# Optimization experiments

Hardware: AMD Instinct MI355X
Metric: run time of the kernel (lower is better)

Reference implementation:

```python
import jax, jax.numpy as jnp
import numpy as np

B, U, F = 32768, 256, 256  # batch, units, input features
LR = 0.01                  # inner_lr
EPS = 1e-3                 # TF LayerNormalization default epsilon


def _layer_norm(x, gamma, beta):
    m = jnp.mean(x, axis=-1, keepdims=True)
    v = jnp.var(x, axis=-1, keepdims=True)
    return (x - m) * jax.lax.rsqrt(v + EPS) * gamma + beta


def _enc(W1, b1, W2, b2, u):
    # mlp_2 inner encoder: Dense(4U, gelu-exact) -> Dense(U)
    return jax.nn.gelu(u @ W1 + b1, approximate=False) @ W2 + b2


def setup_inputs() -> dict:
    key = jax.random.key(0)
    ks = jax.random.split(key, 12)
    def w(k, shape):
        fan_in = shape[0]
        return jax.random.normal(k, shape, jnp.float32) / np.sqrt(fan_in)
    return {
        "x": jax.random.normal(ks[0], (B, F), jnp.float32),
        "h_prev": jax.random.normal(ks[1], (B, U), jnp.float32),
        "W_phi": w(ks[2], (F + U, U)), "b_phi": jnp.zeros((U,), jnp.float32),
        "W_psi": w(ks[3], (F + U, U)), "b_psi": jnp.zeros((U,), jnp.float32),
        "W1": w(ks[4], (U, 4 * U)), "b1": jnp.zeros((4 * U,), jnp.float32),
        "W2": w(ks[5], (4 * U, U)), "b2": jnp.zeros((U,), jnp.float32),
        "W_g": w(ks[6], (U, U)), "g_bias": jnp.zeros((U,), jnp.float32),
        "ln_gamma": jnp.ones((U,), jnp.float32), "ln_beta": jnp.zeros((U,), jnp.float32),
        "W_h": w(ks[7], (U, U)), "h_bias": jnp.zeros((U,), jnp.float32),
    }


def reference(x, h_prev, W_phi, b_phi, W_psi, b_psi, W1, b1, W2, b2,
              W_g, g_bias, ln_gamma, ln_beta, W_h, h_bias):
    z = jnp.concatenate([x, h_prev], axis=-1)          # [B, F+U]
    phi = z @ W_phi + b_phi                            # [B, U], also the inner target

    def inner_loss(params):
        W1_, b1_, W2_, b2_ = params
        r = _enc(W1_, b1_, W2_, b2_, phi) @ W_g + g_bias
        r = _layer_norm(r, ln_gamma, ln_beta)
        return jnp.mean(jnp.square(r - phi)), r

    params = (W1, b1, W2, b2)
    # inner_iterations = 1: one SGD step on the inner-encoder weights only
    (_, recon), grads = jax.value_and_grad(inner_loss, has_aux=True)(params)
    params = tuple(p - LR * g for p, g in zip(params, grads))

    psi = z @ W_psi + b_psi                            # [B, U]
    feat = _enc(*params, psi) + 0.1 * recon            # updated encoder on psi
    out = feat @ W_h + h_bias                          # new hidden / cell output
    return out
```

## Files before the change

### kernel.cpp

```cpp
#include <hip/hip_runtime.h>
#include <math.h>

#define B_N 32768
#define U_N 256
#define H_N 1024
#define LR_C 0.01f
#define EPS_C 1e-3f

typedef unsigned short ushort_t;
typedef unsigned int uint_t;
using frag8 = __attribute__((ext_vector_type(8))) short;
using f32x4 = __attribute__((ext_vector_type(4))) float;

__device__ __forceinline__ float erf_fast(float y) {
    float ay = fabsf(y);
    float t = __builtin_amdgcn_rcpf(fmaf(0.3275911f, ay, 1.0f));
    float p = fmaf(1.061405429f, t, -1.453152027f);
    p = fmaf(p, t, 1.421413741f);
    p = fmaf(p, t, -0.284496736f);
    p = fmaf(p, t, 0.254829592f);
    p = p * t;
    float e = __expf(-ay * ay);
    float r = fmaf(-p, e, 1.0f);
    return copysignf(r, y);
}
__device__ __forceinline__ float gelu_f(float x) {
    return 0.5f * x * (1.0f + erf_fast(x * 0.7071067811865475f));
}
__device__ __forceinline__ float dgelu_f(float x) {
    float c = 0.5f * (1.0f + erf_fast(x * 0.7071067811865475f));
    float p = 0.3989422804014327f * __expf(-0.5f * x * x);
    return fmaf(x, p, c);
}
__device__ __forceinline__ void gelu_pair(float x, float& g, float& d) {
    float ay = fabsf(x) * 0.7071067811865475f;
    float t = __builtin_amdgcn_rcpf(fmaf(0.3275911f, ay, 1.0f));
    float p = fmaf(1.061405429f, t, -1.453152027f);
    p = fmaf(p, t, 1.421413741f);
    p = fmaf(p, t, -0.284496736f);
    p = fmaf(p, t, 0.254829592f);
    p = p * t;
    float e = __expf(-ay * ay);
    float er = copysignf(fmaf(-p, e, 1.0f), x);
    float c = 0.5f * (1.0f + er);
    g = x * c;
    d = fmaf(x * 0.3989422804014327f, e, c);
}
__device__ __forceinline__ void splitf(float v, ushort_t& h, ushort_t& l) {
    uint_t u = __float_as_uint(v);
    h = (ushort_t)(u >> 16);
    float r = v - __uint_as_float(u & 0xFFFF0000u);
    uint_t ru = __float_as_uint(r);
    l = (ushort_t)((ru + 0x7FFFu + ((ru >> 16) & 1u)) >> 16);
}
__device__ __forceinline__ ushort_t cvt_rne(float v) {
    uint_t u = __float_as_uint(v);
    return (ushort_t)((u + 0x7FFFu + ((u >> 16) & 1u)) >> 16);
}
__device__ __forceinline__ float bf2f(ushort_t u) {
    return __uint_as_float((uint_t)u << 16);
}
__device__ __forceinline__ void unpack2(uint_t pa, uint_t pb, uint_t& hw, uint_t& lw) {
    hw = __builtin_amdgcn_perm(pb, pa, 0x07060302u);
    lw = __builtin_amdgcn_perm(pb, pa, 0x05040100u);
}
__device__ __forceinline__ size_t swz(int n, int k, int K) {
    return (size_t)n * K +
           (size_t)((k & ~31) | ((((k >> 3) & 3) ^ ((n >> 1) & 3)) << 3) | (k & 7));
}
__device__ __forceinline__ void gload16(const ushort_t* g, ushort_t* l) {
    __builtin_amdgcn_global_load_lds(
        (const __attribute__((address_space(1))) void*)g,
        (__attribute__((address_space(3))) void*)l, 16, 0, 0);
}

#define EPI_NONE 0
#define EPI_GELU 1
#define EPI_ADDS 3

#define BEP_P   0
#define BEP_PT  1
#define BEP_A1  2
#define BEP_DAT 3

template<int ACONCAT, int APACK, int EPI, int OPACK>
__global__ __launch_bounds__(256)
void mgemm_k(const float* A, const float* A2, const uint_t* __restrict__ AP,
             const ushort_t* __restrict__ BTh, const ushort_t* __restrict__ BTl,
             const float* __restrict__ bias, const ushort_t* __restrict__ Xr,
             float* C, uint_t* Cp,
             int M, int N, int K)
{
    __shared__ ushort_t Ah[128 * 40], Al[128 * 40];
    __shared__ ushort_t Bh[128 * 32], Bl[128 * 32];
    const int tid = threadIdx.x;
    const int m0 = blockIdx.x * 128, n0 = blockIdx.y * 128;
    const int lane = tid & 63, w = tid >> 6;
    const int wm = (w & 1) * 64, wn = (w >> 1) * 64;
    const int fr = lane & 15, fq = lane >> 4;
    const int sr = tid >> 1;
    const int sk = (tid & 1) * 16;

    f32x4 acc[4][4];
    #pragma unroll
    for (int i = 0; i < 4; i++)
        #pragma unroll
        for (int j = 0; j < 4; j++) acc[i][j] = (f32x4){0.f, 0.f, 0.f, 0.f};

    for (int k0 = 0; k0 < K; k0 += 32) {
        {
            const int r0w = w * 32;
            const size_t so = (size_t)(n0 + r0w + (lane >> 2)) * K + k0 + ((lane & 3) << 3);
            gload16(&BTh[so],                  &Bh[r0w * 32]);
            gload16(&BTh[so + (size_t)16 * K], &Bh[(r0w + 16) * 32]);
            gload16(&BTl[so],                  &Bl[r0w * 32]);
            gload16(&BTl[so + (size_t)16 * K], &Bl[(r0w + 16) * 32]);
        }
        if (APACK) {
            const uint_t* ap = AP + (size_t)(m0 + sr) * K + k0 + sk;
            uint4 p0 = *(const uint4*)(ap);
            uint4 p1 = *(const uint4*)(ap + 4);
            uint4 p2 = *(const uint4*)(ap + 8);
            uint4 p3 = *(const uint4*)(ap + 12);
            uint4 h0, h1, l0, l1;
            unpack2(p0.x, p0.y, h0.x, l0.x); unpack2(p0.z, p0.w, h0.y, l0.y);
            unpack2(p1.x, p1.y, h0.z, l0.z); unpack2(p1.z, p1.w, h0.w, l0.w);
            unpack2(p2.x, p2.y, h1.x, l1.x); unpack2(p2.z, p2.w, h1.y, l1.y);
            unpack2(p3.x, p3.y, h1.z, l1.z); unpack2(p3.z, p3.w, h1.w, l1.w);
            *(uint4*)&Ah[sr * 40 + sk]     = h0;
            *(uint4*)&Ah[sr * 40 + sk + 8] = h1;
            *(uint4*)&Al[sr * 40 + sk]     = l0;
            *(uint4*)&Al[sr * 40 + sk + 8] = l1;
        } else {
            #pragma unroll
            for (int g = 0; g < 2; g++) {
                uint4 qh, qa;
                uint_t ph[4], pl[4];
                #pragma unroll
                for (int c = 0; c < 2; c++) {
                    const int ak = k0 + sk + g * 8 + c * 4;
                    const float* ap;
                    if (ACONCAT) ap = (ak < 256) ? (A + (size_t)(m0 + sr) * 256 + ak)
                                                 : (A2 + (size_t)(m0 + sr) * 256 + (ak - 256));
                    else         ap = A + (size_t)(m0 + sr) * K + ak;
                    float4 v = *(const float4*)ap;
                    ushort_t h0,h1,h2,h3,l0,l1,l2,l3;
                    splitf(v.x,h0,l0); splitf(v.y,h1,l1); splitf(v.z,h2,l2); splitf(v.w,h3,l3);
                    ph[c*2]   = (uint_t)h0 | ((uint_t)h1 << 16);
                    ph[c*2+1] = (uint_t)h2 | ((uint_t)h3 << 16);
                    pl[c*2]   = (uint_t)l0 | ((uint_t)l1 << 16);
                    pl[c*2+1] = (uint_t)l2 | ((uint_t)l3 << 16);
                }
                qh.x = ph[0]; qh.y = ph[1]; qh.z = ph[2]; qh.w = ph[3];
                qa.x = pl[0]; qa.y = pl[1]; qa.z = pl[2]; qa.w = pl[3];
                *(uint4*)&Ah[sr * 40 + sk + g * 8] = qh;
                *(uint4*)&Al[sr * 40 + sk + g * 8] = qa;
            }
        }
        __syncthreads();

        frag8 afh[4], afl[4], bfh[4], bfl[4];
        #pragma unroll
        for (int i = 0; i < 4; i++) {
            const int ar = wm + i * 16 + fr;
            afh[i] = *(frag8*)&Ah[ar * 40 + fq * 8];
            afl[i] = *(frag8*)&Al[ar * 40 + fq * 8];
        }
        #pragma unroll
        for (int j = 0; j < 4; j++) {
            const int br = wn + j * 16 + fr;
            const int bs = br * 32 + ((fq ^ ((br >> 1) & 3)) << 3);
            bfh[j] = *(frag8*)&Bh[bs];
            bfl[j] = *(frag8*)&Bl[bs];
        }
        #pragma unroll
        for (int i = 0; i < 4; i++)
            #pragma unroll
            for (int j = 0; j < 4; j++) {
                acc[i][j] = __builtin_amdgcn_mfma_f32_16x16x32_bf16(afh[i], bfh[j], acc[i][j], 0, 0, 0);
                acc[i][j] = __builtin_amdgcn_mfma_f32_16x16x32_bf16(afh[i], bfl[j], acc[i][j], 0, 0, 0);
                acc[i][j] = __builtin_amdgcn_mfma_f32_16x16x32_bf16(afl[i], bfh[j], acc[i][j], 0, 0, 0);
            }
        __syncthreads();
    }

    float bv[4] = {0.f, 0.f, 0.f, 0.f};
    if (bias != nullptr)
        #pragma unroll
        for (int j = 0; j < 4; j++) bv[j] = bias[n0 + wn + j * 16 + fr];
    #pragma unroll
    for (int i = 0; i < 4; i++)
        #pragma unroll
        for (int j = 0; j < 4; j++) {
            const int col = n0 + wn + j * 16 + fr;
            #pragma unroll
            for (int r = 0; r < 4; r++) {
                const int row = m0 + wm + i * 16 + fq * 4 + r;
                const size_t off = (size_t)row * N + col;
                float c = acc[i][j][r] + bv[j];
                if (EPI == EPI_GELU)      c = gelu_f(c);
                else if (EPI == EPI_ADDS) c = c + 0.1f * bf2f(Xr[off]);
                if (OPACK) {
                    ushort_t h, l;
                    splitf(c, h, l);
                    Cp[off] = ((uint_t)h << 16) | (uint_t)l;
                } else {
                    C[off] = c;
                }
            }
        }
}

template<int ACONCAT, int BEP>
__global__ __launch_bounds__(256)
void bgemm_k(const void* Av, const float* A2f, const ushort_t* __restrict__ BTh,
             const float* __restrict__ bias, const ushort_t* __restrict__ GpIn,
             ushort_t* Crm, ushort_t* Cct, ushort_t* GpOut,
             int M, int N, int K)
{
    __shared__ ushort_t Ah[128 * 40];
    __shared__ ushort_t Bh[128 * 32];
    const int tid = threadIdx.x;
    const int m0 = blockIdx.x * 128, n0 = blockIdx.y * 128;
    const int lane = tid & 63, w = tid >> 6;
    const int wm = (w & 1) * 64, wn = (w >> 1) * 64;
    const int fr = lane & 15, fq = lane >> 4;
    const int sr = tid >> 1;
    const int sk = (tid & 1) * 16;

    f32x4 acc[4][4];
    #pragma unroll
    for (int i = 0; i < 4; i++)
        #pragma unroll
        for (int j = 0; j < 4; j++) acc[i][j] = (f32x4){0.f, 0.f, 0.f, 0.f};

    for (int k0 = 0; k0 < K; k0 += 32) {
        {
            const int r0w = w * 32;
            const size_t so = (size_t)(n0 + r0w + (lane >> 2)) * K + k0 + ((lane & 3) << 3);
            gload16(&BTh[so],                  &Bh[r0w * 32]);
            gload16(&BTh[so + (size_t)16 * K], &Bh[(r0w + 16) * 32]);
        }
        if (ACONCAT) {
            const float* A = (const float*)Av;
            #pragma unroll
            for (int g = 0; g < 2; g++) {
                uint_t ph[4];
                #pragma unroll
                for (int c = 0; c < 2; c++) {
                    const int ak = k0 + sk + g * 8 + c * 4;
                    const float* ap = (ak < 256) ? (A + (size_t)(m0 + sr) * 256 + ak)
                                                 : (A2f + (size_t)(m0 + sr) * 256 + (ak - 256));
                    float4 v = *(const float4*)ap;
                    ph[c*2]   = (uint_t)cvt_rne(v.x) | ((uint_t)cvt_rne(v.y) << 16);
                    ph[c*2+1] = (uint_t)cvt_rne(v.z) | ((uint_t)cvt_rne(v.w) << 16);
                }
                uint4 q; q.x = ph[0]; q.y = ph[1]; q.z = ph[2]; q.w = ph[3];
                *(uint4*)&Ah[sr * 40 + sk + g * 8] = q;
            }
        } else {
            const ushort_t* A = (const ushort_t*)Av;
            const size_t ao = (size_t)(m0 + sr) * K + k0 + sk;
            *(uint4*)&Ah[sr * 40 + sk]     = *(const uint4*)&A[ao];
            *(uint4*)&Ah[sr * 40 + sk + 8] = *(const uint4*)&A[ao + 8];
        }
        __syncthreads();

        frag8 af[4], bf[4];
        #pragma unroll
        for (int i = 0; i < 4; i++) af[i] = *(frag8*)&Ah[(wm + i * 16 + fr) * 40 + fq * 8];
        #pragma unroll
        for (int j = 0; j < 4; j++) {
            const int br = wn + j * 16 + fr;
            bf[j] = *(frag8*)&Bh[br * 32 + ((fq ^ ((br >> 1) & 3)) << 3)];
        }
        #pragma unroll
        for (int i = 0; i < 4; i++)
            #pragma unroll
            for (int j = 0; j < 4; j++)
                acc[i][j] = __builtin_amdgcn_mfma_f32_16x16x32_bf16(af[i], bf[j], acc[i][j], 0, 0, 0);
        __syncthreads();
    }

    float bv[4] = {0.f, 0.f, 0.f, 0.f};
    if (bias != nullptr)
        #pragma unroll
        for (int j = 0; j < 4; j++) bv[j] = bias[n0 + wn + j * 16 + fr];
    #pragma unroll
    for (int i = 0; i < 4; i++)
        #pragma unroll
        for (int j = 0; j < 4; j++) {
            const int col = n0 + wn + j * 16 + fr;
            const int rowb = m0 + wm + i * 16 + fq * 4;
            float v[4];
            #pragma unroll
            for (int r = 0; r < 4; r++) v[r] = acc[i][j][r] + bv[j];
            if (BEP == BEP_A1) {
                ushort_t gc[4];
                #pragma unroll
                for (int r = 0; r < 4; r++) {
                    float g, d;
                    gelu_pair(v[r], g, d);
                    gc[r] = cvt_rne(g);
                    Crm[(size_t)(rowb + r) * N + col] = gc[r];
                    GpOut[(size_t)(rowb + r) * N + col] = cvt_rne(d);
                }
                uint_t p0 = (uint_t)gc[0] | ((uint_t)gc[1] << 16);
                uint_t p1 = (uint_t)gc[2] | ((uint_t)gc[3] << 16);
                *(uint2*)&Cct[(size_t)col * M + rowb] = (uint2){p0, p1};
            } else if (BEP == BEP_DAT) {
                ushort_t dc[4];
                #pragma unroll
                for (int r = 0; r < 4; r++)
                    dc[r] = cvt_rne(v[r] * bf2f(GpIn[(size_t)(rowb + r) * N + col]));
                uint_t p0 = (uint_t)dc[0] | ((uint_t)dc[1] << 16);
                uint_t p1 = (uint_t)dc[2] | ((uint_t)dc[3] << 16);
                *(uint2*)&Cct[(size_t)col * M + rowb] = (uint2){p0, p1};
            } else {
                ushort_t cc[4];
                #pragma unroll
                for (int r = 0; r < 4; r++) {
                    cc[r] = cvt_rne(v[r]);
                    Crm[(size_t)(rowb + r) * N + col] = cc[r];
                }
                if (BEP == BEP_PT) {
                    uint_t p0 = (uint_t)cc[0] | ((uint_t)cc[1] << 16);
                    uint_t p1 = (uint_t)cc[2] | ((uint_t)cc[3] << 16);
                    *(uint2*)&Cct[(size_t)col * M + rowb] = (uint2){p0, p1};
                }
            }
        }
}

__global__ __launch_bounds__(256)
void wgrad_k(const ushort_t* __restrict__ AT, const ushort_t* __restrict__ BTt,
             float* C, int M, int N, int KA, int kofsA, int KB, int kofsB, int KC)
{
    __shared__ ushort_t Ah[128 * 40];
    __shared__ ushort_t Bh[128 * 40];
    const int tid = threadIdx.x;
    const int m0 = blockIdx.x * 128, n0 = blockIdx.y * 128;
    const int kbA = kofsA + blockIdx.z * KC;
    const int kbB = kofsB + blockIdx.z * KC;
    const int lane = tid & 63, w = tid >> 6;
    const int wm = (w & 1) * 64, wn = (w >> 1) * 64;
    const int fr = lane & 15, fq = lane >> 4;
    const int sr = tid >> 1;
    const int sk = (tid & 1) * 16;

    f32x4 acc[4][4];
    #pragma unroll
    for (int i = 0; i < 4; i++)
        #pragma unroll
        for (int j = 0; j < 4; j++) acc[i][j] = (f32x4){0.f, 0.f, 0.f, 0.f};

    for (int k0 = 0; k0 < KC; k0 += 32) {
        const size_t ao = (size_t)(m0 + sr) * KA + kbA + k0 + sk;
        *(uint4*)&Ah[sr * 40 + sk]     = *(const uint4*)&AT[ao];
        *(uint4*)&Ah[sr * 40 + sk + 8] = *(const uint4*)&AT[ao + 8];
        const size_t bo = (size_t)(n0 + sr) * KB + kbB + k0 + sk;
        *(uint4*)&Bh[sr * 40 + sk]     = *(const uint4*)&BTt[bo];
        *(uint4*)&Bh[sr * 40 + sk + 8] = *(const uint4*)&BTt[bo + 8];
        __syncthreads();

        frag8 af[4], bf[4];
        #pragma unroll
        for (int i = 0; i < 4; i++) af[i] = *(frag8*)&Ah[(wm + i * 16 + fr) * 40 + fq * 8];
        #pragma unroll
        for (int j = 0; j < 4; j++) bf[j] = *(frag8*)&Bh[(wn + j * 16 + fr) * 40 + fq * 8];
        #pragma unroll
        for (int i = 0; i < 4; i++)
            #pragma unroll
            for (int j = 0; j < 4; j++)
                acc[i][j] = __builtin_amdgcn_mfma_f32_16x16x32_bf16(af[i], bf[j], acc[i][j], 0, 0, 0);
        __syncthreads();
    }
    #pragma unroll
    for (int i = 0; i < 4; i++)
        #pragma unroll
        for (int j = 0; j < 4; j++) {
            const int col = n0 + wn + j * 16 + fr;
            #pragma unroll
            for (int r = 0; r < 4; r++) {
                const int row = m0 + wm + i * 16 + fq * 4 + r;
                atomicAdd(&C[(size_t)row * N + col], acc[i][j][r]);
            }
        }
}

__global__ __launch_bounds__(256)
void colsumT_k(const ushort_t* __restrict__ T, float* db, int LD, int cols)
{
    const int n = blockIdx.x * 4 + (threadIdx.x >> 6);
    const int lane = threadIdx.x & 63;
    const ushort_t* row = T + (size_t)n * LD;
    float s = 0.f;
    for (int c = lane * 8; c < cols; c += 512) {
        uint4 q = *(const uint4*)&row[c];
        uint_t u[4] = {q.x, q.y, q.z, q.w};
        #pragma unroll
        for (int t = 0; t < 4; t++) {
            s += bf2f((ushort_t)(u[t] & 0xFFFF));
            s += bf2f((ushort_t)(u[t] >> 16));
        }
    }
    #pragma unroll
    for (int o = 32; o > 0; o >>= 1) s += __shfl_xor(s, o);
    if (lane == 0) atomicAdd(&db[n], s);
}

__global__ __launch_bounds__(256)
void ln_bf_k(const ushort_t* r0, const ushort_t* __restrict__ phi,
             const float* __restrict__ gamma, const float* __restrict__ beta,
             ushort_t* recon, ushort_t* dr0)
{
    const int lane = threadIdx.x & 63;
    const int wv = threadIdx.x >> 6;
    const int row = blockIdx.x * 4 + wv;
    const size_t base = (size_t)row * U_N + (lane << 2);

    uint2 xu = *(const uint2*)(r0 + base);
    uint2 pu = *(const uint2*)(phi + base);
    float xs[4] = { bf2f((ushort_t)(xu.x & 0xFFFF)), bf2f((ushort_t)(xu.x >> 16)),
                    bf2f((ushort_t)(xu.y & 0xFFFF)), bf2f((ushort_t)(xu.y >> 16)) };
    float ps[4] = { bf2f((ushort_t)(pu.x & 0xFFFF)), bf2f((ushort_t)(pu.x >> 16)),
                    bf2f((ushort_t)(pu.y & 0xFFFF)), bf2f((ushort_t)(pu.y >> 16)) };
    float s = xs[0] + xs[1] + xs[2] + xs[3];
    float sq = xs[0]*xs[0] + xs[1]*xs[1] + xs[2]*xs[2] + xs[3]*xs[3];
    #pragma unroll
    for (int o = 32; o > 0; o >>= 1) { s += __shfl_xor(s, o); sq += __shfl_xor(sq, o); }
    const float m   = s * (1.0f / U_N);
    const float var = sq * (1.0f / U_N) - m * m;
    const float inv = rsqrtf(var + EPS_C);

    float4 gv = *(const float4*)(gamma + (lane << 2));
    float4 bvv = *(const float4*)(beta + (lane << 2));
    float gs[4] = {gv.x, gv.y, gv.z, gv.w};
    float bs[4] = {bvv.x, bvv.y, bvv.z, bvv.w};
    float rh[4], dh[4], rc[4];
    float s1 = 0.f, s2 = 0.f;
    const float gscale = 2.0f / ((float)B_N * (float)U_N);
    #pragma unroll
    for (int j = 0; j < 4; j++) {
        rh[j] = (xs[j] - m) * inv;
        rc[j] = rh[j] * gs[j] + bs[j];
        float g2 = gscale * (rc[j] - ps[j]);
        dh[j] = g2 * gs[j];
        s1 += dh[j];
        s2 += dh[j] * rh[j];
    }
    #pragma unroll
    for (int o = 32; o > 0; o >>= 1) { s1 += __shfl_xor(s1, o); s2 += __shfl_xor(s2, o); }
    const float mu1 = s1 * (1.0f / U_N);
    const float mu2 = s2 * (1.0f / U_N);
    ushort_t oc[4], dc[4];
    #pragma unroll
    for (int j = 0; j < 4; j++) {
        oc[j] = cvt_rne(rc[j]);
        dc[j] = cvt_rne(inv * (dh[j] - mu1 - rh[j] * mu2));
    }
    *(uint2*)(recon + base) = (uint2){ (uint_t)oc[0] | ((uint_t)oc[1] << 16),
                                       (uint_t)oc[2] | ((uint_t)oc[3] << 16) };
    *(uint2*)(dr0 + base)   = (uint2){ (uint_t)dc[0] | ((uint_t)dc[1] << 16),
                                       (uint_t)dc[2] | ((uint_t)dc[3] << 16) };
}

template<int HASL>
__global__ __launch_bounds__(256)
void tsplit_k(const float* __restrict__ W, ushort_t* __restrict__ Th,
              ushort_t* __restrict__ Tl, int R, int C)
{
    __shared__ float t[64][65];
    const int tid = threadIdx.x;
    const int R0 = blockIdx.x * 64, C0 = blockIdx.y * 64;
    const int c = tid & 63, rb = (tid >> 6) * 16;
    for (int i = 0; i < 16; i++)
        t[rb + i][c] = W[(size_t)(R0 + rb + i) * C + C0 + c];
    __syncthreads();
    const int orr = tid & 63, ob = (tid >> 6) * 16;
    for (int i = 0; i < 16; i++) {
        const int oc = ob + i;
        ushort_t h, l;
        splitf(t[orr][oc], h, l);
        const size_t d = swz(C0 + oc, R0 + orr, R);
        Th[d] = h;
        if (HASL) Tl[d] = l;
    }
}

__global__ __launch_bounds__(256)
void tupd_k(const float* __restrict__ W, const float* __restrict__ dW,
            ushort_t* __restrict__ Th, ushort_t* __restrict__ Tl, int R, int C)
{
    __shared__ float t[64][65];
    const int tid = threadIdx.x;
    const int R0 = blockIdx.x * 64, C0 = blockIdx.y * 64;
    const int c = tid & 63, rb = (tid >> 6) * 16;
    for (int i = 0; i < 16; i++) {
        const size_t o = (size_t)(R0 + rb + i) * C + C0 + c;
        t[rb + i][c] = W[o] - LR_C * dW[o];
    }
    __syncthreads();
    const int orr = tid & 63, ob = (tid >> 6) * 16;
    for (int i = 0; i < 16; i++) {
        const int oc = ob + i;
        ushort_t h, l;
        splitf(t[orr][oc], h, l);
        const size_t d = swz(C0 + oc, R0 + orr, R);
        Th[d] = h;
        Tl[d] = l;
    }
}

__global__ __launch_bounds__(256)
void scvt_k(const float* __restrict__ W, ushort_t* __restrict__ Th, int n4)
{
    const int i = blockIdx.x * 256 + threadIdx.x;
    if (i >= n4) return;
    float4 v = *(const float4*)(W + (size_t)i * 4);
    const int f = i * 4;
    const int row = f >> 8, col = f & 255;
    uint2 ph;
    ph.x = (uint_t)cvt_rne(v.x) | ((uint_t)cvt_rne(v.y) << 16);
    ph.y = (uint_t)cvt_rne(v.z) | ((uint_t)cvt_rne(v.w) << 16);
    *(uint2*)&Th[swz(row, col, 256)] = ph;
}

__global__ __launch_bounds__(256)
void bupd_k(const float* __restrict__ b1, const float* __restrict__ db1,
            const float* __restrict__ b2, const float* __restrict__ db2,
            float* __restrict__ b1u, float* __restrict__ b2u)
{
    const int i = blockIdx.x * 256 + threadIdx.x;
    if (i < H_N) b1u[i] = b1[i] - LR_C * db1[i];
    else if (i < H_N + U_N) b2u[i - H_N] = b2[i - H_N] - LR_C * db2[i - H_N];
}

extern "C" void kernel_launch(void* const* d_in, const int* in_sizes, int n_in,
                              void* d_out, int out_size, void* d_ws, size_t ws_size,
                              hipStream_t stream)
{
    const float* x      = (const float*)d_in[0];
    const float* h_prev = (const float*)d_in[1];
    const float* W_phi  = (const float*)d_in[2];
    const float* b_phi  = (const float*)d_in[3];
    const float* W_psi  = (const float*)d_in[4];
    const float* b_psi  = (const float*)d_in[5];
    const float* W1     = (const float*)d_in[6];
    const float* b1     = (const float*)d_in[7];
    const float* W2     = (const float*)d_in[8];
    const float* b2     = (const float*)d_in[9];
    const float* W_g    = (const float*)d_in[10];
    const float* g_bias = (const float*)d_in[11];
    const float* gamma  = (const float*)d_in[12];
    const float* beta   = (const float*)d_in[13];
    const float* W_h    = (const float*)d_in[14];
    const float* h_bias = (const float*)d_in[15];
    float* out = (float*)d_out;

    const size_t BU = (size_t)B_N * U_N;
    const size_t UH = (size_t)U_N * H_N;

    float* ws  = (float*)d_ws;
    float* dW1 = ws;
    float* db1 = dW1 + UH;
    float* dW2 = db1 + H_N;
    float* db2 = dW2 + UH;
    float* b1u = db2 + U_N;
    float* b2u = b1u + H_N;
    ushort_t* us = (ushort_t*)(((uintptr_t)(b2u + U_N) + 15) & ~(uintptr_t)15);
    ushort_t* WphiT_h = us;
    ushort_t* WpsiT_h = WphiT_h + 131072;     ushort_t* WpsiT_l = WpsiT_h + 131072;
    ushort_t* W1T_h   = WpsiT_l + 131072;
    ushort_t* W2T_h   = W1T_h + 262144;
    ushort_t* W2s_h   = W2T_h + 262144;
    ushort_t* Wgs_h   = W2s_h + 262144;
    ushort_t* WgT_h   = Wgs_h + 65536;
    ushort_t* W1uT_h  = WgT_h + 65536;        ushort_t* W1uT_l = W1uT_h + 262144;
    ushort_t* W2uT_h  = W1uT_l + 262144;      ushort_t* W2uT_l = W2uT_h + 262144;
    ushort_t* WhT_h   = W2uT_l + 262144;      ushort_t* WhT_l  = WhT_h + 65536;
    ushort_t* phi_bf  = WhT_l + 65536;
    ushort_t* phiT_bf = phi_bf + BU;
    ushort_t* recon_bf= phiT_bf + BU;
    ushort_t* chunk0  = recon_bf + BU;
    const size_t P_bytes = (size_t)((char*)chunk0 - (char*)d_ws);

    int GA = 2;
    while (GA < 256 && P_bytes + (size_t)(B_N / GA) * 10240 + (1 << 20) > ws_size) GA *= 2;
    size_t region = (size_t)(B_N / GA) * 10240;
    int GC = 1;
    while (GC < 256) {
        size_t cC = (size_t)(B_N / GC) * 6144;
        size_t r = cC > region ? cC : region;
        if (P_bytes + r + (1 << 20) <= ws_size) { region = r; break; }
        GC *= 2;
    }
    const int BcA = B_N / GA;
    const int BcC = B_N / GC;
    const int KC = (BcA >= 8192) ? 512 : ((BcA >= 1024) ? BcA / 16 : BcA);
    const int Z  = BcA / KC;

    ushort_t* g1  = chunk0;
    ushort_t* gp  = g1  + (size_t)BcA * H_N;
    ushort_t* g1T = gp  + (size_t)BcA * H_N;
    ushort_t* daT = g1T + (size_t)BcA * H_N;
    ushort_t* e_b = daT + (size_t)BcA * H_N;
    ushort_t* r0b = e_b + (size_t)BcA * U_N;
    ushort_t* deb = r0b + (size_t)BcA * U_N;
    ushort_t* deT = deb + (size_t)BcA * U_N;
    uint_t* psi_p  = (uint_t*)chunk0;
    uint_t* h2_p   = psi_p + (size_t)BcC * U_N;
    uint_t* feat_p = h2_p  + (size_t)BcC * H_N;

    hipMemsetAsync(dW1, 0, (2 * UH + H_N + U_N) * sizeof(float), stream);

    dim3 blk(256);
    tsplit_k<0><<<dim3(8, 4),  blk, 0, stream>>>(W_phi, WphiT_h, nullptr, 512, 256);
    tsplit_k<1><<<dim3(8, 4),  blk, 0, stream>>>(W_psi, WpsiT_h, WpsiT_l, 512, 256);
    tsplit_k<0><<<dim3(4, 16), blk, 0, stream>>>(W1, W1T_h, nullptr, 256, 1024);
    tsplit_k<0><<<dim3(16, 4), blk, 0, stream>>>(W2, W2T_h, nullptr, 1024, 256);
    tsplit_k<0><<<dim3(4, 4),  blk, 0, stream>>>(W_g, WgT_h, nullptr, 256, 256);
    tsplit_k<1><<<dim3(4, 4),  blk, 0, stream>>>(W_h, WhT_h, WhT_l, 256, 256);
    scvt_k<<<dim3(256), blk, 0, stream>>>(W2, W2s_h, 65536);
    scvt_k<<<dim3(64),  blk, 0, stream>>>(W_g, Wgs_h, 16384);

    bgemm_k<1, BEP_PT><<<dim3(B_N / 128, 2), blk, 0, stream>>>(
        x, h_prev, WphiT_h, b_phi, nullptr, phi_bf, phiT_bf, nullptr, B_N, U_N, 512);

    for (int c = 0; c < GA; c++) {
        const size_t off = (size_t)c * BcA;
        const ushort_t* phic = phi_bf + off * U_N;
        bgemm_k<0, BEP_A1><<<dim3(BcA / 128, 8), blk, 0, stream>>>(
            phic, nullptr, W1T_h, b1, nullptr, g1, g1T, gp, BcA, H_N, U_N);
        bgemm_k<0, BEP_P><<<dim3(BcA / 128, 2), blk, 0, stream>>>(
            g1, nullptr, W2T_h, b2, nullptr, e_b, nullptr, nullptr, BcA, U_N, H_N);
        bgemm_k<0, BEP_P><<<dim3(BcA / 128, 2), blk, 0, stream>>>(
            e_b, nullptr, WgT_h, g_bias, nullptr, r0b, nullptr, nullptr, BcA, U_N, U_N);
        ln_bf_k<<<dim3(BcA / 4), blk, 0, stream>>>(r0b, phic, gamma, beta,
                                                   recon_bf + off * U_N, r0b);
        bgemm_k<0, BEP_PT><<<dim3(BcA / 128, 2), blk, 0, stream>>>(
            r0b, nullptr, Wgs_h, nullptr, nullptr, deb, deT, nullptr, BcA, U_N, U_N);
        bgemm_k<0, BEP_DAT><<<dim3(BcA / 128, 8), blk, 0, stream>>>(
            deb, nullptr, W2s_h, nullptr, gp, nullptr, daT, nullptr, BcA, H_N, U_N);
        wgrad_k<<<dim3(8, 2, Z), blk, 0, stream>>>(g1T, deT, dW2, H_N, U_N,
                                                   BcA, 0, BcA, 0, KC);
        colsumT_k<<<dim3(U_N / 4), blk, 0, stream>>>(deT, db2, BcA, BcA);
        wgrad_k<<<dim3(2, 8, Z), blk, 0, stream>>>(phiT_bf, daT, dW1, U_N, H_N,
                                                   B_N, (int)off, BcA, 0, KC);
        colsumT_k<<<dim3(H_N / 4), blk, 0, stream>>>(daT, db1, BcA, BcA);
    }

    bupd_k<<<dim3(5), blk, 0, stream>>>(b1, db1, b2, db2, b1u, b2u);
    tupd_k<<<dim3(4, 16), blk, 0, stream>>>(W1, dW1, W1uT_h, W1uT_l, 256, 1024);
    tupd_k<<<dim3(16, 4), blk, 0, stream>>>(W2, dW2, W2uT_h, W2uT_l, 1024, 256);

    for (int c = 0; c < GC; c++) {
        const size_t off = (size_t)c * BcC;
        mgemm_k<1, 0, EPI_NONE, 1><<<dim3(BcC / 128, 2), blk, 0, stream>>>(
            x + off * 256, h_prev + off * U_N, nullptr,
            WpsiT_h, WpsiT_l, b_psi, nullptr,
            nullptr, psi_p, BcC, U_N, 512);
        mgemm_k<0, 1, EPI_GELU, 1><<<dim3(BcC / 128, 8), blk, 0, stream>>>(
            nullptr, nullptr, psi_p,
            W1uT_h, W1uT_l, b1u, nullptr,
            nullptr, h2_p, BcC, H_N, U_N);
        mgemm_k<0, 1, EPI_ADDS, 1><<<dim3(BcC / 128, 2), blk, 0, stream>>>(
            nullptr, nullptr, h2_p,
            W2uT_h, W2uT_l, b2u, recon_bf + off * U_N,
            nullptr, feat_p, BcC, U_N, H_N);
        mgemm_k<0, 1, EPI_NONE, 0><<<dim3(BcC / 128, 2), blk, 0, stream>>>(
            nullptr, nullptr, feat_p,
            WhT_h, WhT_l, h_bias, nullptr,
            out + off * U_N, nullptr, BcC, U_N, U_N);
    }
}
```

Baseline: 873.6 us.

## Load MFMA fragments directly from global memory, bypassing LDS staging

GEMM kernels whose A operand is already bf16 or packed (bgemm, mgemm and wgrad variants) now read MFMA fragments straight from global memory into registers, dropping the LDS tiles and __syncthreads barriers. The concat/float-input GEMMs keep LDS staging as separate kernels. Weight layouts consumed by the direct kernels are written unswizzled to match plain row indexing. This removes LDS traffic and barrier stalls but gives up cross-wave operand sharing through LDS, so each wave issues redundant global/L2 loads with strided 16-byte accesses.

Measured after the change: 1.091 ms. +24.9%, slower.

```diff
diff --git a/kernel.cpp b/kernel.cpp
--- a/kernel.cpp
+++ b/kernel.cpp
@@ -26,11 +26,6 @@
 }
 __device__ __forceinline__ float gelu_f(float x) {
     return 0.5f * x * (1.0f + erf_fast(x * 0.7071067811865475f));
-}
-__device__ __forceinline__ float dgelu_f(float x) {
-    float c = 0.5f * (1.0f + erf_fast(x * 0.7071067811865475f));
-    float p = 0.3989422804014327f * __expf(-0.5f * x * x);
-    return fmaf(x, p, c);
 }
 __device__ __forceinline__ void gelu_pair(float x, float& g, float& d) {
     float ay = fabsf(x) * 0.7071067811865475f;
@@ -83,23 +78,19 @@
 #define BEP_A1  2
 #define BEP_DAT 3
 
-template<int ACONCAT, int APACK, int EPI, int OPACK>
-__global__ __launch_bounds__(256)
-void mgemm_k(const float* A, const float* A2, const uint_t* __restrict__ AP,
+template<int EPI, int OPACK>
+__global__ __launch_bounds__(256)
+void mgemm_d(const uint_t* __restrict__ AP,
              const ushort_t* __restrict__ BTh, const ushort_t* __restrict__ BTl,
              const float* __restrict__ bias, const ushort_t* __restrict__ Xr,
              float* C, uint_t* Cp,
              int M, int N, int K)
 {
-    __shared__ ushort_t Ah[128 * 40], Al[128 * 40];
-    __shared__ ushort_t Bh[128 * 32], Bl[128 * 32];
     const int tid = threadIdx.x;
     const int m0 = blockIdx.x * 128, n0 = blockIdx.y * 128;
     const int lane = tid & 63, w = tid >> 6;
     const int wm = (w & 1) * 64, wn = (w >> 1) * 64;
     const int fr = lane & 15, fq = lane >> 4;
-    const int sr = tid >> 1;
-    const int sk = (tid & 1) * 16;
 
     f32x4 acc[4][4];
     #pragma unroll
@@ -108,70 +99,23 @@
         for (int j = 0; j < 4; j++) acc[i][j] = (f32x4){0.f, 0.f, 0.f, 0.f};
 
     for (int k0 = 0; k0 < K; k0 += 32) {
-        {
-            const int r0w = w * 32;
-            const size_t so = (size_t)(n0 + r0w + (lane >> 2)) * K + k0 + ((lane & 3) << 3);
-            gload16(&BTh[so],                  &Bh[r0w * 32]);
-            gload16(&BTh[so + (size_t)16 * K], &Bh[(r0w + 16) * 32]);
-            gload16(&BTl[so],                  &Bl[r0w * 32]);
-            gload16(&BTl[so + (size_t)16 * K], &Bl[(r0w + 16) * 32]);
-        }
-        if (APACK) {
-            const uint_t* ap = AP + (size_t)(m0 + sr) * K + k0 + sk;
-            uint4 p0 = *(const uint4*)(ap);
+        frag8 afh[4], afl[4], bfh[4], bfl[4];
+        #pragma unroll
+        for (int i = 0; i < 4; i++) {
+            const uint_t* ap = AP + (size_t)(m0 + wm + i * 16 + fr) * K + k0 + fq * 8;
+            uint4 p0 = *(const uint4*)ap;
             uint4 p1 = *(const uint4*)(ap + 4);
-            uint4 p2 = *(const uint4*)(ap + 8);
-            uint4 p3 = *(const uint4*)(ap + 12);
-            uint4 h0, h1, l0, l1;
-            unpack2(p0.x, p0.y, h0.x, l0.x); unpack2(p0.z, p0.w, h0.y, l0.y);
-            unpack2(p1.x, p1.y, h0.z, l0.z); unpack2(p1.z, p1.w, h0.w, l0.w);
-            unpack2(p2.x, p2.y, h1.x, l1.x); unpack2(p2.z, p2.w, h1.y, l1.y);
-            unpack2(p3.x, p3.y, h1.z, l1.z); unpack2(p3.z, p3.w, h1.w, l1.w);
-            *(uint4*)&Ah[sr * 40 + sk]     = h0;
-            *(uint4*)&Ah[sr * 40 + sk + 8] = h1;
-            *(uint4*)&Al[sr * 40 + sk]     = l0;
-            *(uint4*)&Al[sr * 40 + sk + 8] = l1;
-        } else {
-            #pragma unroll
-            for (int g = 0; g < 2; g++) {
-                uint4 qh, qa;
-                uint_t ph[4], pl[4];
-                #pragma unroll
-                for (int c = 0; c < 2; c++) {
-                    const int ak = k0 + sk + g * 8 + c * 4;
-                    const float* ap;
-                    if (ACONCAT) ap = (ak < 256) ? (A + (size_t)(m0 + sr) * 256 + ak)
-                                                 : (A2 + (size_t)(m0 + sr) * 256 + (ak - 256));
-                    else         ap = A + (size_t)(m0 + sr) * K + ak;
-                    float4 v = *(const float4*)ap;
-                    ushort_t h0,h1,h2,h3,l0,l1,l2,l3;
-                    splitf(v.x,h0,l0); splitf(v.y,h1,l1); splitf(v.z,h2,l2); splitf(v.w,h3,l3);
-                    ph[c*2]   = (uint_t)h0 | ((uint_t)h1 << 16);
-                    ph[c*2+1] = (uint_t)h2 | ((uint_t)h3 << 16);
-                    pl[c*2]   = (uint_t)l0 | ((uint_t)l1 << 16);
-                    pl[c*2+1] = (uint_t)l2 | ((uint_t)l3 << 16);
-                }
-                qh.x = ph[0]; qh.y = ph[1]; qh.z = ph[2]; qh.w = ph[3];
-                qa.x = pl[0]; qa.y = pl[1]; qa.z = pl[2]; qa.w = pl[3];
-                *(uint4*)&Ah[sr * 40 + sk + g * 8] = qh;
-                *(uint4*)&Al[sr * 40 + sk + g * 8] = qa;
-            }
-        }
-        __syncthreads();
-
-        frag8 afh[4], afl[4], bfh[4], bfl[4];
-        #pragma unroll
-        for (int i = 0; i < 4; i++) {
-            const int ar = wm + i * 16 + fr;
-            afh[i] = *(frag8*)&Ah[ar * 40 + fq * 8];
-            afl[i] = *(frag8*)&Al[ar * 40 + fq * 8];
+            uint4 h, l;
+            unpack2(p0.x, p0.y, h.x, l.x); unpack2(p0.z, p0.w, h.y, l.y);
+            unpack2(p1.x, p1.y, h.z, l.z); unpack2(p1.z, p1.w, h.w, l.w);
+            afh[i] = *(frag8*)&h;
+            afl[i] = *(frag8*)&l;
         }
         #pragma unroll
         for (int j = 0; j < 4; j++) {
-            const int br = wn + j * 16 + fr;
-            const int bs = br * 32 + ((fq ^ ((br >> 1) & 3)) << 3);
-            bfh[j] = *(frag8*)&Bh[bs];
-            bfl[j] = *(frag8*)&Bl[bs];
+            const size_t bo = (size_t)(n0 + wn + j * 16 + fr) * K + k0 + fq * 8;
+            bfh[j] = *(const frag8*)&BTh[bo];
+            bfl[j] = *(const frag8*)&BTl[bo];
         }
         #pragma unroll
         for (int i = 0; i < 4; i++)
@@ -181,7 +125,6 @@
                 acc[i][j] = __builtin_amdgcn_mfma_f32_16x16x32_bf16(afh[i], bfl[j], acc[i][j], 0, 0, 0);
                 acc[i][j] = __builtin_amdgcn_mfma_f32_16x16x32_bf16(afl[i], bfh[j], acc[i][j], 0, 0, 0);
             }
-        __syncthreads();
     }
 
     float bv[4] = {0.f, 0.f, 0.f, 0.f};
@@ -195,7 +138,7 @@
             const int col = n0 + wn + j * 16 + fr;
             #pragma unroll
             for (int r = 0; r < 4; r++) {
-                const int row = m0 + wm + i * 16 + fq * 4 + r;
+                const int row = m0 + wm + i * 16 + (lane >> 4) * 4 + r;
                 const size_t off = (size_t)row * N + col;
                 float c = acc[i][j][r] + bv[j];
                 if (EPI == EPI_GELU)      c = gelu_f(c);
@@ -211,15 +154,16 @@
         }
 }
 
-template<int ACONCAT, int BEP>
-__global__ __launch_bounds__(256)
-void bgemm_k(const void* Av, const float* A2f, const ushort_t* __restrict__ BTh,
-             const float* __restrict__ bias, const ushort_t* __restrict__ GpIn,
-             ushort_t* Crm, ushort_t* Cct, ushort_t* GpOut,
+template<int OPACK>
+__global__ __launch_bounds__(256)
+void mgemm_c(const float* A, const float* A2,
+             const ushort_t* __restrict__ BTh, const ushort_t* __restrict__ BTl,
+             const float* __restrict__ bias,
+             float* C, uint_t* Cp,
              int M, int N, int K)
 {
-    __shared__ ushort_t Ah[128 * 40];
-    __shared__ ushort_t Bh[128 * 32];
+    __shared__ ushort_t Ah[128 * 40], Al[128 * 40];
+    __shared__ ushort_t Bh[128 * 32], Bl[128 * 32];
     const int tid = threadIdx.x;
     const int m0 = blockIdx.x * 128, n0 = blockIdx.y * 128;
     const int lane = tid & 63, w = tid >> 6;
@@ -240,46 +184,115 @@
             const size_t so = (size_t)(n0 + r0w + (lane >> 2)) * K + k0 + ((lane & 3) << 3);
             gload16(&BTh[so],                  &Bh[r0w * 32]);
             gload16(&BTh[so + (size_t)16 * K], &Bh[(r0w + 16) * 32]);
-        }
-        if (ACONCAT) {
-            const float* A = (const float*)Av;
-            #pragma unroll
-            for (int g = 0; g < 2; g++) {
-                uint_t ph[4];
-                #pragma unroll
-                for (int c = 0; c < 2; c++) {
-                    const int ak = k0 + sk + g * 8 + c * 4;
-                    const float* ap = (ak < 256) ? (A + (size_t)(m0 + sr) * 256 + ak)
-                                                 : (A2f + (size_t)(m0 + sr) * 256 + (ak - 256));
-                    float4 v = *(const float4*)ap;
-                    ph[c*2]   = (uint_t)cvt_rne(v.x) | ((uint_t)cvt_rne(v.y) << 16);
-                    ph[c*2+1] = (uint_t)cvt_rne(v.z) | ((uint_t)cvt_rne(v.w) << 16);
-                }
-                uint4 q; q.x = ph[0]; q.y = ph[1]; q.z = ph[2]; q.w = ph[3];
-                *(uint4*)&Ah[sr * 40 + sk + g * 8] = q;
-            }
-        } else {
-            const ushort_t* A = (const ushort_t*)Av;
-            const size_t ao = (size_t)(m0 + sr) * K + k0 + sk;
-            *(uint4*)&Ah[sr * 40 + sk]     = *(const uint4*)&A[ao];
-            *(uint4*)&Ah[sr * 40 + sk + 8] = *(const uint4*)&A[ao + 8];
+            gload16(&BTl[so],                  &Bl[r0w * 32]);
+            gload16(&BTl[so + (size_t)16 * K], &Bl[(r0w + 16) * 32]);
+        }
+        #pragma unroll
+        for (int g = 0; g < 2; g++) {
+            uint4 qh, qa;
+            uint_t ph[4], pl[4];
+            #pragma unroll
+            for (int c = 0; c < 2; c++) {
+                const int ak = k0 + sk + g * 8 + c * 4;
+                const float* ap = (ak < 256) ? (A + (size_t)(m0 + sr) * 256 + ak)
+                                             : (A2 + (size_t)(m0 + sr) * 256 + (ak - 256));
+                float4 v = *(const float4*)ap;
+                ushort_t h0,h1,h2,h3,l0,l1,l2,l3;
+                splitf(v.x,h0,l0); splitf(v.y,h1,l1); splitf(v.z,h2,l2); splitf(v.w,h3,l3);
+                ph[c*2]   = (uint_t)h0 | ((uint_t)h1 << 16);
+                ph[c*2+1] = (uint_t)h2 | ((uint_t)h3 << 16);
+                pl[c*2]   = (uint_t)l0 | ((uint_t)l1 << 16);
+                pl[c*2+1] = (uint_t)l2 | ((uint_t)l3 << 16);
+            }
+            qh.x = ph[0]; qh.y = ph[1]; qh.z = ph[2]; qh.w = ph[3];
+            qa.x = pl[0]; qa.y = pl[1]; qa.z = pl[2]; qa.w = pl[3];
+            *(uint4*)&Ah[sr * 40 + sk + g * 8] = qh;
+            *(uint4*)&Al[sr * 40 + sk + g * 8] = qa;
         }
         __syncthreads();
 
-        frag8 af[4], bf[4];
-        #pragma unroll
-        for (int i = 0; i < 4; i++) af[i] = *(frag8*)&Ah[(wm + i * 16 + fr) * 40 + fq * 8];
+        frag8 afh[4], afl[4], bfh[4], bfl[4];
+        #pragma unroll
+        for (int i = 0; i < 4; i++) {
+            const int ar = wm + i * 16 + fr;
+            afh[i] = *(frag8*)&Ah[ar * 40 + fq * 8];
+            afl[i] = *(frag8*)&Al[ar * 40 + fq * 8];
+        }
         #pragma unroll
         for (int j = 0; j < 4; j++) {
             const int br = wn + j * 16 + fr;
-            bf[j] = *(frag8*)&Bh[br * 32 + ((fq ^ ((br >> 1) & 3)) << 3)];
-        }
+            const int bs = br * 32 + ((fq ^ ((br >> 1) & 3)) << 3);
+            bfh[j] = *(frag8*)&Bh[bs];
+            bfl[j] = *(frag8*)&Bl[bs];
+        }
+        #pragma unroll
+        for (int i = 0; i < 4; i++)
+            #pragma unroll
+            for (int j = 0; j < 4; j++) {
+                acc[i][j] = __builtin_amdgcn_mfma_f32_16x16x32_bf16(afh[i], bfh[j], acc[i][j], 0, 0, 0);
+                acc[i][j] = __builtin_amdgcn_mfma_f32_16x16x32_bf16(afh[i], bfl[j], acc[i][j], 0, 0, 0);
+                acc[i][j] = __builtin_amdgcn_mfma_f32_16x16x32_bf16(afl[i], bfh[j], acc[i][j], 0, 0, 0);
+            }
+        __syncthreads();
+    }
+
+    float bv[4] = {0.f, 0.f, 0.f, 0.f};
+    if (bias != nullptr)
+        #pragma unroll
+        for (int j = 0; j < 4; j++) bv[j] = bias[n0 + wn + j * 16 + fr];
+    #pragma unroll
+    for (int i = 0; i < 4; i++)
+        #pragma unroll
+        for (int j = 0; j < 4; j++) {
+            const int col = n0 + wn + j * 16 + fr;
+            #pragma unroll
+            for (int r = 0; r < 4; r++) {
+                const int row = m0 + wm + i * 16 + fq * 4 + r;
+                const size_t off = (size_t)row * N + col;
+                float c = acc[i][j][r] + bv[j];
+                if (OPACK) {
+                    ushort_t h, l;
+                    splitf(c, h, l);
+                    Cp[off] = ((uint_t)h << 16) | (uint_t)l;
+                } else {
+                    C[off] = c;
+                }
+            }
+        }
+}
+
+template<int BEP>
+__global__ __launch_bounds__(256)
+void bgemm_d(const ushort_t* __restrict__ A, const ushort_t* __restrict__ BTh,
+             const float* __restrict__ bias, const ushort_t* __restrict__ GpIn,
+             ushort_t* Crm, ushort_t* Cct, ushort_t* GpOut,
+             int M, int N, int K)
+{
+    const int tid = threadIdx.x;
+    const int m0 = blockIdx.x * 128, n0 = blockIdx.y * 128;
+    const int lane = tid & 63, w = tid >> 6;
+    const int wm = (w & 1) * 64, wn = (w >> 1) * 64;
+    const int fr = lane & 15, fq = lane >> 4;
+
+    f32x4 acc[4][4];
+    #pragma unroll
+    for (int i = 0; i < 4; i++)
+        #pragma unroll
+        for (int j = 0; j < 4; j++) acc[i][j] = (f32x4){0.f, 0.f, 0.f, 0.f};
+
+    for (int k0 = 0; k0 < K; k0 += 32) {
+        frag8 af[4], bf[4];
+        #pragma unroll
+        for (int i = 0; i < 4; i++)
+            af[i] = *(const frag8*)&A[(size_t)(m0 + wm + i * 16 + fr) * K + k0 + fq * 8];
+        #pragma unroll
+        for (int j = 0; j < 4; j++)
+            bf[j] = *(const frag8*)&BTh[(size_t)(n0 + wn + j * 16 + fr) * K + k0 + fq * 8];
         #pragma unroll
         for (int i = 0; i < 4; i++)
             #pragma unroll
             for (int j = 0; j < 4; j++)
                 acc[i][j] = __builtin_amdgcn_mfma_f32_16x16x32_bf16(af[i], bf[j], acc[i][j], 0, 0, 0);
-        __syncthreads();
     }
 
     float bv[4] = {0.f, 0.f, 0.f, 0.f};
@@ -332,12 +345,97 @@
         }
 }
 
+template<int BEP>
+__global__ __launch_bounds__(256)
+void bgemm_c(const float* A, const float* A2f, const ushort_t* __restrict__ BTh,
+             const float* __restrict__ bias,
+             ushort_t* Crm, ushort_t* Cct,
+             int M, int N, int K)
+{
+    __shared__ ushort_t Ah[128 * 40];
+    __shared__ ushort_t Bh[128 * 32];
+    const int tid = threadIdx.x;
+    const int m0 = blockIdx.x * 128, n0 = blockIdx.y * 128;
+    const int lane = tid & 63, w = tid >> 6;
+    const int wm = (w & 1) * 64, wn = (w >> 1) * 64;
+    const int fr = lane & 15, fq = lane >> 4;
+    const int sr = tid >> 1;
+    const int sk = (tid & 1) * 16;
+
+    f32x4 acc[4][4];
+    #pragma unroll
+    for (int i = 0; i < 4; i++)
+        #pragma unroll
+        for (int j = 0; j < 4; j++) acc[i][j] = (f32x4){0.f, 0.f, 0.f, 0.f};
+
+    for (int k0 = 0; k0 < K; k0 += 32) {
+        {
+            const int r0w = w * 32;
+            const size_t so = (size_t)(n0 + r0w + (lane >> 2)) * K + k0 + ((lane & 3) << 3);
+            gload16(&BTh[so],                  &Bh[r0w * 32]);
+            gload16(&BTh[so + (size_t)16 * K], &Bh[(r0w + 16) * 32]);
+        }
+        #pragma unroll
+        for (int g = 0; g < 2; g++) {
+            uint_t ph[4];
+            #pragma unroll
+            for (int c = 0; c < 2; c++) {
+                const int ak = k0 + sk + g * 8 + c * 4;
+                const float* ap = (ak < 256) ? (A + (size_t)(m0 + sr) * 256 + ak)
+                                             : (A2f + (size_t)(m0 + sr) * 256 + (ak - 256));
+                float4 v = *(const float4*)ap;
+                ph[c*2]   = (uint_t)cvt_rne(v.x) | ((uint_t)cvt_rne(v.y) << 16);
+                ph[c*2+1] = (uint_t)cvt_rne(v.z) | ((uint_t)cvt_rne(v.w) << 16);
+            }
+            uint4 q; q.x = ph[0]; q.y = ph[1]; q.z = ph[2]; q.w = ph[3];
+            *(uint4*)&Ah[sr * 40 + sk + g * 8] = q;
+        }
+        __syncthreads();
+
+        frag8 af[4], bf[4];
+        #pragma unroll
+        for (int i = 0; i < 4; i++) af[i] = *(frag8*)&Ah[(wm + i * 16 + fr) * 40 + fq * 8];
+        #pragma unroll
+        for (int j = 0; j < 4; j++) {
+            const int br = wn + j * 16 + fr;
+            bf[j] = *(frag8*)&Bh[br * 32 + ((fq ^ ((br >> 1) & 3)) << 3)];
+        }
+        #pragma unroll
+        for (int i = 0; i < 4; i++)
+            #pragma unroll
+            for (int j = 0; j < 4; j++)
+                acc[i][j] = __builtin_amdgcn_mfma_f32_16x16x32_bf16(af[i], bf[j], acc[i][j], 0, 0, 0);
+        __syncthreads();
+    }
+
+    float bv[4] = {0.f, 0.f, 0.f, 0.f};
+    if (bias != nullptr)
+        #pragma unroll
+        for (int j = 0; j < 4; j++) bv[j] = bias[n0 + wn + j * 16 + fr];
+    #pragma unroll
+    for (int i = 0; i < 4; i++)
+        #pragma unroll
+        for (int j = 0; j < 4; j++) {
+            const int col = n0 + wn + j * 16 + fr;
+            const int rowb = m0 + wm + i * 16 + fq * 4;
+            ushort_t cc[4];
+            #pragma unroll
+            for (int r = 0; r < 4; r++) {
+                cc[r] = cvt_rne(acc[i][j][r] + bv[j]);
+                Crm[(size_t)(rowb + r) * N + col] = cc[r];
+            }
+            if (BEP == BEP_PT) {
+                uint_t p0 = (uint_t)cc[0] | ((uint_t)cc[1] << 16);
+                uint_t p1 = (uint_t)cc[2] | ((uint_t)cc[3] << 16);
+                *(uint2*)&Cct[(size_t)col * M + rowb] = (uint2){p0, p1};
+            }
+        }
+}
+
 __global__ __launch_bounds__(256)
 void wgrad_k(const ushort_t* __restrict__ AT, const ushort_t* __restrict__ BTt,
              float* C, int M, int N, int KA, int kofsA, int KB, int kofsB, int KC)
 {
-    __shared__ ushort_t Ah[128 * 40];
-    __shared__ ushort_t Bh[128 * 40];
     const int tid = threadIdx.x;
     const int m0 = blockIdx.x * 128, n0 = blockIdx.y * 128;
     const int kbA = kofsA + blockIdx.z * KC;
@@ -345,8 +443,6 @@
     const int lane = tid & 63, w = tid >> 6;
     const int wm = (w & 1) * 64, wn = (w >> 1) * 64;
     const int fr = lane & 15, fq = lane >> 4;
-    const int sr = tid >> 1;
-    const int sk = (tid & 1) * 16;
 
     f32x4 acc[4][4];
     #pragma unroll
@@ -355,25 +451,18 @@
         for (int j = 0; j < 4; j++) acc[i][j] = (f32x4){0.f, 0.f, 0.f, 0.f};
 
     for (int k0 = 0; k0 < KC; k0 += 32) {
-        const size_t ao = (size_t)(m0 + sr) * KA + kbA + k0 + sk;
-        *(uint4*)&Ah[sr * 40 + sk]     = *(const uint4*)&AT[ao];
-        *(uint4*)&Ah[sr * 40 + sk + 8] = *(const uint4*)&AT[ao + 8];
-        const size_t bo = (size_t)(n0 + sr) * KB + kbB + k0 + sk;
-        *(uint4*)&Bh[sr * 40 + sk]     = *(const uint4*)&BTt[bo];
-        *(uint4*)&Bh[sr * 40 + sk + 8] = *(const uint4*)&BTt[bo + 8];
-        __syncthreads();
-
         frag8 af[4], bf[4];
         #pragma unroll
-        for (int i = 0; i < 4; i++) af[i] = *(frag8*)&Ah[(wm + i * 16 + fr) * 40 + fq * 8];
-        #pragma unroll
-        for (int j = 0; j < 4; j++) bf[j] = *(frag8*)&Bh[(wn + j * 16 + fr) * 40 + fq * 8];
+        for (int i = 0; i < 4; i++)
+            af[i] = *(const frag8*)&AT[(size_t)(m0 + wm + i * 16 + fr) * KA + kbA + k0 + fq * 8];
+        #pragma unroll
+        for (int j = 0; j < 4; j++)
+            bf[j] = *(const frag8*)&BTt[(size_t)(n0 + wn + j * 16 + fr) * KB + kbB + k0 + fq * 8];
         #pragma unroll
         for (int i = 0; i < 4; i++)
             #pragma unroll
             for (int j = 0; j < 4; j++)
                 acc[i][j] = __builtin_amdgcn_mfma_f32_16x16x32_bf16(af[i], bf[j], acc[i][j], 0, 0, 0);
-        __syncthreads();
     }
     #pragma unroll
     for (int i = 0; i < 4; i++)
@@ -465,7 +554,7 @@
                                        (uint_t)dc[2] | ((uint_t)dc[3] << 16) };
 }
 
-template<int HASL>
+template<int HASL, int SWZ>
 __global__ __launch_bounds__(256)
 void tsplit_k(const float* __restrict__ W, ushort_t* __restrict__ Th,
               ushort_t* __restrict__ Tl, int R, int C)
@@ -482,7 +571,8 @@
         const int oc = ob + i;
         ushort_t h, l;
         splitf(t[orr][oc], h, l);
-        const size_t d = swz(C0 + oc, R0 + orr, R);
+        const size_t d = SWZ ? swz(C0 + oc, R0 + orr, R)
+                             : (size_t)(C0 + oc) * R + R0 + orr;
         Th[d] = h;
         if (HASL) Tl[d] = l;
     }
@@ -506,9 +596,8 @@
         const int oc = ob + i;
         ushort_t h, l;
         splitf(t[orr][oc], h, l);
-        const size_t d = swz(C0 + oc, R0 + orr, R);
-        Th[d] = h;
-        Tl[d] = l;
+        Th[(size_t)(C0 + oc) * R + R0 + orr] = h;
+        Tl[(size_t)(C0 + oc) * R + R0 + orr] = l;
     }
 }
 
@@ -518,12 +607,10 @@
     const int i = blockIdx.x * 256 + threadIdx.x;
     if (i >= n4) return;
     float4 v = *(const float4*)(W + (size_t)i * 4);
-    const int f = i * 4;
-    const int row = f >> 8, col = f & 255;
     uint2 ph;
     ph.x = (uint_t)cvt_rne(v.x) | ((uint_t)cvt_rne(v.y) << 16);
     ph.y = (uint_t)cvt_rne(v.z) | ((uint_t)cvt_rne(v.w) << 16);
-    *(uint2*)&Th[swz(row, col, 256)] = ph;
+    *(uint2*)&Th[(size_t)i * 4] = ph;
 }
 
 __global__ __launch_bounds__(256)
@@ -615,33 +702,33 @@
     hipMemsetAsync(dW1, 0, (2 * UH + H_N + U_N) * sizeof(float), stream);
 
     dim3 blk(256);
-    tsplit_k<0><<<dim3(8, 4),  blk, 0, stream>>>(W_phi, WphiT_h, nullptr, 512, 256);
-    tsplit_k<1><<<dim3(8, 4),  blk, 0, stream>>>(W_psi, WpsiT_h, WpsiT_l, 512, 256);
-    tsplit_k<0><<<dim3(4, 16), blk, 0, stream>>>(W1, W1T_h, nullptr, 256, 1024);
-    tsplit_k<0><<<dim3(16, 4), blk, 0, stream>>>(W2, W2T_h, nullptr, 1024, 256);
-    tsplit_k<0><<<dim3(4, 4),  blk, 0, stream>>>(W_g, WgT_h, nullptr, 256, 256);
-    tsplit_k<1><<<dim3(4, 4),  blk, 0, stream>>>(W_h, WhT_h, WhT_l, 256, 256);
+    tsplit_k<0,1><<<dim3(8, 4),  blk, 0, stream>>>(W_phi, WphiT_h, nullptr, 512, 256);
+    tsplit_k<1,1><<<dim3(8, 4),  blk, 0, stream>>>(W_psi, WpsiT_h, WpsiT_l, 512, 256);
+    tsplit_k<0,0><<<dim3(4, 16), blk, 0, stream>>>(W1, W1T_h, nullptr, 256, 1024);
+    tsplit_k<0,0><<<dim3(16, 4), blk, 0, stream>>>(W2, W2T_h, nullptr, 1024, 256);
+    tsplit_k<0,0><<<dim3(4, 4),  blk, 0, stream>>>(W_g, WgT_h, nullptr, 256, 256);
+    tsplit_k<1,0><<<dim3(4, 4),  blk, 0, stream>>>(W_h, WhT_h, WhT_l, 256, 256);
     scvt_k<<<dim3(256), blk, 0, stream>>>(W2, W2s_h, 65536);
     scvt_k<<<dim3(64),  blk, 0, stream>>>(W_g, Wgs_h, 16384);
 
-    bgemm_k<1, BEP_PT><<<dim3(B_N / 128, 2), blk, 0, stream>>>(
-        x, h_prev, WphiT_h, b_phi, nullptr, phi_bf, phiT_bf, nullptr, B_N, U_N, 512);
+    bgemm_c<BEP_PT><<<dim3(B_N / 128, 2), blk, 0, stream>>>(
+        x, h_prev, WphiT_h, b_phi, phi_bf, phiT_bf, B_N, U_N, 512);
 
     for (int c = 0; c < GA; c++) {
         const size_t off = (size_t)c * BcA;
         const ushort_t* phic = phi_bf + off * U_N;
-        bgemm_k<0, BEP_A1><<<dim3(BcA / 128, 8), blk, 0, stream>>>(
-            phic, nullptr, W1T_h, b1, nullptr, g1, g1T, gp, BcA, H_N, U_N);
-        bgemm_k<0, BEP_P><<<dim3(BcA / 128, 2), blk, 0, stream>>>(
-            g1, nullptr, W2T_h, b2, nullptr, e_b, nullptr, nullptr, BcA, U_N, H_N);
-        bgemm_k<0, BEP_P><<<dim3(BcA / 128, 2), blk, 0, stream>>>(
-            e_b, nullptr, WgT_h, g_bias, nullptr, r0b, nullptr, nullptr, BcA, U_N, U_N);
+        bgemm_d<BEP_A1><<<dim3(BcA / 128, 8), blk, 0, stream>>>(
+            phic, W1T_h, b1, nullptr, g1, g1T, gp, BcA, H_N, U_N);
+        bgemm_d<BEP_P><<<dim3(BcA / 128, 2), blk, 0, stream>>>(
+            g1, W2T_h, b2, nullptr, e_b, nullptr, nullptr, BcA, U_N, H_N);
+        bgemm_d<BEP_P><<<dim3(BcA / 128, 2), blk, 0, stream>>>(
+            e_b, WgT_h, g_bias, nullptr, r0b, nullptr, nullptr, BcA, U_N, U_N);
         ln_bf_k<<<dim3(BcA / 4), blk, 0, stream>>>(r0b, phic, gamma, beta,
                                                    recon_bf + off * U_N, r0b);
-        bgemm_k<0, BEP_PT><<<dim3(BcA / 128, 2), blk, 0, stream>>>(
-            r0b, nullptr, Wgs_h, nullptr, nullptr, deb, deT, nullptr, BcA, U_N, U_N);
-        bgemm_k<0, BEP_DAT><<<dim3(BcA / 128, 8), blk, 0, stream>>>(
-            deb, nullptr, W2s_h, nullptr, gp, nullptr, daT, nullptr, BcA, H_N, U_N);
+        bgemm_d<BEP_PT><<<dim3(BcA / 128, 2), blk, 0, stream>>>(
+            r0b, Wgs_h, nullptr, nullptr, deb, deT, nullptr, BcA, U_N, U_N);
+        bgemm_d<BEP_DAT><<<dim3(BcA / 128, 8), blk, 0, stream>>>(
+            deb, W2s_h, nullptr, gp, nullptr, daT, nullptr, BcA, H_N, U_N);
         wgrad_k<<<dim3(8, 2, Z), blk, 0, stream>>>(g1T, deT, dW2, H_N, U_N,
                                                    BcA, 0, BcA, 0, KC);
         colsumT_k<<<dim3(U_N / 4), blk, 0, stream>>>(deT, db2, BcA, BcA);
@@ -656,21 +743,18 @@
 
     for (int c = 0; c < GC; c++) {
         const size_t off = (size_t)c * BcC;
-        mgemm_k<1, 0, EPI_NONE, 1><<<dim3(BcC / 128, 2), blk, 0, stream>>>(
-            x + off * 256, h_prev + off * U_N, nullptr,
-            WpsiT_h, WpsiT_l, b_psi, nullptr,
+        mgemm_c<1><<<dim3(BcC / 128, 2), blk, 0, stream>>>(
+            x + off * 256, h_prev + off * U_N,
+            WpsiT_h, WpsiT_l, b_psi,
             nullptr, psi_p, BcC, U_N, 512);
-        mgemm_k<0, 1, EPI_GELU, 1><<<dim3(BcC / 128, 8), blk, 0, stream>>>(
-            nullptr, nullptr, psi_p,
-            W1uT_h, W1uT_l, b1u, nullptr,
+        mgemm_d<EPI_GELU, 1><<<dim3(BcC / 128, 8), blk, 0, stream>>>(
+            psi_p, W1uT_h, W1uT_l, b1u, nullptr,
             nullptr, h2_p, BcC, H_N, U_N);
-        mgemm_k<0, 1, EPI_ADDS, 1><<<dim3(BcC / 128, 2), blk, 0, stream>>>(
-            nullptr, nullptr, h2_p,
-            W2uT_h, W2uT_l, b2u, recon_bf + off * U_N,
+        mgemm_d<EPI_ADDS, 1><<<dim3(BcC / 128, 2), blk, 0, stream>>>(
+            h2_p, W2uT_h, W2uT_l, b2u, recon_bf + off * U_N,
             nullptr, feat_p, BcC, U_N, H_N);
-        mgemm_k<0, 1, EPI_NONE, 0><<<dim3(BcC / 128, 2), blk, 0, stream>>>(
-            nullptr, nullptr, feat_p,
-            WhT_h, WhT_l, h_bias, nullptr,
+        mgemm_d<EPI_NONE, 0><<<dim3(BcC / 128, 2), blk, 0, stream>>>(
+            feat_p, WhT_h, WhT_l, h_bias, nullptr,
             out + off * U_N, nullptr, BcC, U_N, U_N);
     }
 }
```
